# Kernel optimization log

Hardware: AMD Instinct MI355X
Metric: run time of the kernel (lower is better)

## Reference

```python
import jax, jax.numpy as jnp
import numpy as np

HIDDEN = 128
EDGE_DIM = 64
N_NODES = 50000
N_EDGES = 600000

def _linear_params(key, fan_in, fan_out):
    kw, kb = jax.random.split(key)
    bound = 1.0 / np.sqrt(fan_in)
    W = jax.random.uniform(kw, (fan_in, fan_out), minval=-bound, maxval=bound, dtype=jnp.float32)
    b = jax.random.uniform(kb, (fan_out,), minval=-bound, maxval=bound, dtype=jnp.float32)
    return W, b

def setup_inputs() -> dict:
    key = jax.random.key(0)
    ks = jax.random.split(key, 10)
    h = jax.random.normal(ks[0], (N_NODES, HIDDEN), dtype=jnp.float32)
    edge_index = jax.random.randint(ks[1], (2, N_EDGES), 0, N_NODES, dtype=jnp.int64)
    edge_attr = jax.random.normal(ks[2], (N_EDGES, EDGE_DIM), dtype=jnp.float32)
    mW1, mb1 = _linear_params(ks[3], 2 * HIDDEN + EDGE_DIM, HIDDEN)
    mW2, mb2 = _linear_params(ks[4], HIDDEN, HIDDEN)
    mW3, mb3 = _linear_params(ks[5], HIDDEN, HIDDEN)
    uW1, ub1 = _linear_params(ks[6], 2 * HIDDEN, HIDDEN)
    uW2, ub2 = _linear_params(ks[7], HIDDEN, HIDDEN)
    gamma = jnp.ones((HIDDEN,), dtype=jnp.float32)
    beta = jnp.zeros((HIDDEN,), dtype=jnp.float32)
    return {"h": h, "edge_index": edge_index, "edge_attr": edge_attr,
            "mW1": mW1, "mb1": mb1, "mW2": mW2, "mb2": mb2, "mW3": mW3, "mb3": mb3,
            "uW1": uW1, "ub1": ub1, "uW2": uW2, "ub2": ub2,
            "gamma": gamma, "beta": beta}

def reference(h, edge_index, edge_attr, mW1, mb1, mW2, mb2, mW3, mb3, uW1, ub1, uW2, ub2, gamma, beta):
    src, dst = edge_index[0], edge_index[1]
    # message MLP on [E, 2*H + edge_dim]
    x = jnp.concatenate([h[src], h[dst], edge_attr], axis=-1)
    x = jax.nn.gelu(x @ mW1 + mb1)
    x = jax.nn.gelu(x @ mW2 + mb2)
    msgs = x @ mW3 + mb3  # [E, H]
    # scatter-mean aggregate to destination nodes
    agg = jax.ops.segment_sum(msgs, dst, num_segments=h.shape[0])
    count = jax.ops.segment_sum(jnp.ones((dst.shape[0], 1), dtype=h.dtype), dst, num_segments=h.shape[0])
    agg = agg / (count + 1e-8)
    # update MLP
    u = jnp.concatenate([h, agg], axis=-1)
    u = jax.nn.gelu(u @ uW1 + ub1)
    out = u @ uW2 + ub2
    # LayerNorm(out + h)
    y = out + h
    mu = jnp.mean(y, axis=-1, keepdims=True)
    var = jnp.var(y, axis=-1, keepdims=True)
    return (y - mu) / jnp.sqrt(var + 1e-5) * gamma + beta
```

## Files before the change

kernel.cpp:

```cpp
#include <hip/hip_runtime.h>

#define E_TOTAL 600000
#define NN 50000

typedef _Float16 half8 __attribute__((ext_vector_type(8)));
typedef _Float16 half2v __attribute__((ext_vector_type(2)));
typedef float float4v __attribute__((ext_vector_type(4)));
typedef float float2v __attribute__((ext_vector_type(2)));

__device__ __forceinline__ float gelu_tanh(float x) {
    float u = 0.7978845608028654f * (x + 0.044715f * x * x * x);
    float ex = __expf(2.0f * u);
    float t = 1.0f - 2.0f / (ex + 1.0f);
    return 0.5f * x * (1.0f + t);
}

__device__ __forceinline__ int act_idx(int c, int row, int q) {
    int idx = ((c * 128 + row) << 3) + q;
    idx ^= ((row >> 3) & 3) << 4;
    idx ^= (c & 1) << 3;
    return idx;
}
__device__ __forceinline__ int act_idx64(int c, int row, int q) {
    int idx = ((c * 64 + row) << 3) + q;
    idx ^= ((row >> 3) & 3) << 4;
    idx ^= (c & 1) << 3;
    return idx;
}

__device__ __forceinline__ half8 cvt8(float4v x0, float4v x1) {
    half8 a;
    a[0] = (_Float16)x0[0]; a[1] = (_Float16)x0[1]; a[2] = (_Float16)x0[2]; a[3] = (_Float16)x0[3];
    a[4] = (_Float16)x1[0]; a[5] = (_Float16)x1[1]; a[6] = (_Float16)x1[2]; a[7] = (_Float16)x1[3];
    return a;
}

__global__ __launch_bounds__(256) void pack_all(
    const float* __restrict__ mW1, const float* __restrict__ mW2, const float* __restrict__ mW3,
    const float* __restrict__ uW1, const float* __restrict__ uW2,
    _Float16* __restrict__ dst)
{
    int t = blockIdx.x * 256 + threadIdx.x;
    const float* src;
    int loc;
    if (t < 40960)        { src = mW1; loc = t; }
    else if (t < 57344)   { src = mW2; loc = t - 40960; }
    else if (t < 73728)   { src = mW3; loc = t - 57344; }
    else if (t < 106496)  { src = uW1; loc = t - 73728; }
    else if (t < 122880)  { src = uW2; loc = t - 106496; }
    else return;
    int i   = loc & 7;
    int col = (loc >> 3) & 127;
    int c   = loc >> 10;
    dst[t] = (_Float16)src[(8 * c + i) * 128 + col];
}

__global__ __launch_bounds__(256) void cvt_pre(
    const float* __restrict__ h, _Float16* __restrict__ hf)
{
    const int stride = gridDim.x * 256;
    for (int i = blockIdx.x * 256 + threadIdx.x; i < 800000; i += stride) {
        float4v a = ((const float4v*)h)[2 * i];
        float4v b = ((const float4v*)h)[2 * i + 1];
        ((half8*)hf)[i] = cvt8(a, b);
    }
}

__device__ __forceinline__ int detect_i64(const int* ei) {
    int allz = 1;
    #pragma unroll
    for (int j = 1; j < 64; j += 2) allz &= (ei[j] == 0);
    return allz;
}

__global__ __launch_bounds__(256) void count_kernel(const int* __restrict__ ei, int* __restrict__ cnt_i) {
    __shared__ int s_mode;
    if (threadIdx.x == 0) s_mode = detect_i64(ei);
    __syncthreads();
    int e = blockIdx.x * 256 + threadIdx.x;
    if (e >= E_TOTAL) return;
    int d = s_mode ? (int)((const long long*)ei)[E_TOTAL + e] : ei[E_TOTAL + e];
    atomicAdd(&cnt_i[d], 1);
}

__global__ __launch_bounds__(1024) void scan_kernel(const int* __restrict__ cnt_i, int* __restrict__ offs) {
    __shared__ int part[1024];
    const int t = threadIdx.x;
    const int PER = (NN + 1023) / 1024;
    const int base = t * PER;
    int s = 0;
    for (int j = 0; j < PER; ++j) { int idx = base + j; if (idx < NN) s += cnt_i[idx]; }
    part[t] = s;
    __syncthreads();
    for (int off = 1; off < 1024; off <<= 1) {
        int v = (t >= off) ? part[t - off] : 0;
        __syncthreads();
        part[t] += v;
        __syncthreads();
    }
    int run = (t == 0) ? 0 : part[t - 1];
    for (int j = 0; j < PER; ++j) { int idx = base + j; if (idx < NN) { offs[idx] = run; run += cnt_i[idx]; } }
    if (t == 1023) offs[NN] = part[1023];
}

__global__ __launch_bounds__(256) void fill_kernel(const int* __restrict__ ei, const int* __restrict__ offs,
                                                   int* __restrict__ cursor, int* __restrict__ perm) {
    __shared__ int s_mode;
    if (threadIdx.x == 0) s_mode = detect_i64(ei);
    __syncthreads();
    int e = blockIdx.x * 256 + threadIdx.x;
    if (e >= E_TOTAL) return;
    int d = s_mode ? (int)((const long long*)ei)[E_TOTAL + e] : ei[E_TOTAL + e];
    int pos = offs[d] + atomicAdd(&cursor[d], 1);
    perm[pos] = e;
}

__global__ __launch_bounds__(256) void agg_kernel(const _Float16* __restrict__ msgs,
                                                  const int* __restrict__ offs,
                                                  float* __restrict__ agg, float* __restrict__ cntf) {
    const int node = blockIdx.x * 4 + (threadIdx.x >> 6);
    const int l = threadIdx.x & 63;
    const int beg = offs[node], end = offs[node + 1];
    float2v s = {0.0f, 0.0f};
    const half2v* p = (const half2v*)msgs + (size_t)beg * 64 + l;
    int j = beg;
    for (; j + 3 < end; j += 4, p += 256) {
        half2v a = __builtin_nontemporal_load(p);
        half2v b = __builtin_nontemporal_load(p + 64);
        half2v c = __builtin_nontemporal_load(p + 128);
        half2v d = __builtin_nontemporal_load(p + 192);
        s.x += (float)a[0] + (float)b[0] + (float)c[0] + (float)d[0];
        s.y += (float)a[1] + (float)b[1] + (float)c[1] + (float)d[1];
    }
    for (; j < end; ++j, p += 64) {
        half2v v = __builtin_nontemporal_load(p);
        s.x += (float)v[0]; s.y += (float)v[1];
    }
    ((float2v*)agg)[(size_t)node * 64 + l] = s;
    if (l == 0) cntf[node] = (float)(end - beg);
}

template<int ATOMIC>
__global__ __launch_bounds__(128, 3) void msg_kernel(
    const _Float16* __restrict__ hf16, const int* __restrict__ ei, const float* __restrict__ eattr,
    const int* __restrict__ perm,
    const _Float16* __restrict__ pw1, const _Float16* __restrict__ pw2, const _Float16* __restrict__ pw3,
    const float* __restrict__ mb1, const float* __restrict__ mb2, const float* __restrict__ mb3,
    _Float16* __restrict__ msgs, float* __restrict__ agg, float* __restrict__ cnt)
{
    __shared__ int s_e[64];
    __shared__ int s_src[64];
    __shared__ int s_dst[64];
    __shared__ int s_mode;
    __shared__ __align__(16) _Float16 s_act[16 * 64 * 8];

    const int tid = threadIdx.x;
    const int e0  = blockIdx.x * 64;

    if (tid == 0) s_mode = detect_i64(ei);
    __syncthreads();

    if (tid < 64) {
        int e = perm[e0 + tid];
        s_e[tid] = e;
        int srcn, dstn;
        if (s_mode) {
            const long long* e64 = (const long long*)ei;
            srcn = (int)e64[e];
            dstn = (int)e64[E_TOTAL + e];
        } else {
            srcn = ei[e];
            dstn = ei[E_TOTAL + e];
        }
        s_src[tid] = srcn;
        s_dst[tid] = dstn;
        if (ATOMIC) unsafeAtomicAdd(&cnt[dstn], 1.0f);
    }
    __syncthreads();

    const int w = tid >> 6, l = tid & 63, lhi = l >> 4, llo = l & 15;
    const int r0 = 32 * w;
    const float4v fzero = {0.0f, 0.0f, 0.0f, 0.0f};

    const _Float16* srcP[2];
    const _Float16* dstP[2];
    const float*    eP[2];
    #pragma unroll
    for (int ms = 0; ms < 2; ++ms) {
        const int row = r0 + 16 * ms + llo;
        srcP[ms] = hf16 + (size_t)s_src[row] * 128 + 8 * lhi;
        dstP[ms] = hf16 + (size_t)s_dst[row] * 128 + 8 * lhi;
        eP[ms]   = eattr + (size_t)s_e[row] * 64 + 8 * lhi;
    }

    float4v acc[2][8];
    #pragma unroll
    for (int ms = 0; ms < 2; ++ms)
        #pragma unroll
        for (int t = 0; t < 8; ++t) acc[ms][t] = fzero;

    half8 af[4][2];
    #pragma unroll
    for (int s = 0; s < 4; ++s)
        #pragma unroll
        for (int ms = 0; ms < 2; ++ms)
            af[s][ms] = *(const half8*)(srcP[ms] + 32 * s);

    #pragma unroll
    for (int s = 0; s < 10; ++s) {
        const int bbase = ((4 * s + lhi) * 128 + llo) << 3;
        #pragma unroll
        for (int t = 0; t < 8; ++t) {
            const half8 b = *(const half8*)(pw1 + bbase + (t << 7));
            acc[0][t] = __builtin_amdgcn_mfma_f32_16x16x32_f16(af[s & 3][0], b, acc[0][t], 0, 0, 0);
            acc[1][t] = __builtin_amdgcn_mfma_f32_16x16x32_f16(af[s & 3][1], b, acc[1][t], 0, 0, 0);
        }
        if (s + 4 <= 9) {
            const int sn = s + 4;
            #pragma unroll
            for (int ms = 0; ms < 2; ++ms) {
                if (sn < 8) {
                    af[sn & 3][ms] = *(const half8*)(dstP[ms] + 32 * (sn - 4));
                } else {
                    const float* p = eP[ms] + 32 * (sn - 8);
                    float4v x0 = *(const float4v*)p;
                    float4v x1 = *(const float4v*)(p + 4);
                    af[sn & 3][ms] = cvt8(x0, x1);
                }
            }
        }
    }

    #pragma unroll
    for (int t = 0; t < 8; ++t) {
        const int col = 16 * t + llo;
        const float b1 = mb1[col];
        #pragma unroll
        for (int ms = 0; ms < 2; ++ms)
            #pragma unroll
            for (int i = 0; i < 4; ++i) {
                const int row = r0 + 16 * ms + 4 * lhi + i;
                float v = gelu_tanh(acc[ms][t][i] + b1);
                s_act[act_idx64(col >> 3, row, col & 7)] = (_Float16)v;
            }
    }

    float4v acc2[2][8];
    #pragma unroll
    for (int ms = 0; ms < 2; ++ms)
        #pragma unroll
        for (int t = 0; t < 8; ++t) acc2[ms][t] = fzero;

    #pragma unroll
    for (int s = 0; s < 4; ++s) {
        half8 a2[2];
        #pragma unroll
        for (int ms = 0; ms < 2; ++ms)
            a2[ms] = *(const half8*)&s_act[act_idx64(4 * s + lhi, r0 + 16 * ms + llo, 0)];
        const int bbase = ((4 * s + lhi) * 128 + llo) << 3;
        #pragma unroll
        for (int t = 0; t < 8; ++t) {
            const half8 b = *(const half8*)(pw2 + bbase + (t << 7));
            acc2[0][t] = __builtin_amdgcn_mfma_f32_16x16x32_f16(a2[0], b, acc2[0][t], 0, 0, 0);
            acc2[1][t] = __builtin_amdgcn_mfma_f32_16x16x32_f16(a2[1], b, acc2[1][t], 0, 0, 0);
        }
    }

    #pragma unroll
    for (int t = 0; t < 8; ++t) {
        const int col = 16 * t + llo;
        const float b2 = mb2[col];
        #pragma unroll
        for (int ms = 0; ms < 2; ++ms)
            #pragma unroll
            for (int i = 0; i < 4; ++i) {
                const int row = r0 + 16 * ms + 4 * lhi + i;
                float v = gelu_tanh(acc2[ms][t][i] + b2);
                s_act[act_idx64(col >> 3, row, col & 7)] = (_Float16)v;
            }
    }

    float4v acc3[2][8];
    #pragma unroll
    for (int ms = 0; ms < 2; ++ms)
        #pragma unroll
        for (int t = 0; t < 8; ++t) acc3[ms][t] = fzero;

    #pragma unroll
    for (int s = 0; s < 4; ++s) {
        half8 a3[2];
        #pragma unroll
        for (int ms = 0; ms < 2; ++ms)
            a3[ms] = *(const half8*)&s_act[act_idx64(4 * s + lhi, r0 + 16 * ms + llo, 0)];
        const int bbase = ((4 * s + lhi) * 128 + llo) << 3;
        #pragma unroll
        for (int t = 0; t < 8; ++t) {
            const half8 b = *(const half8*)(pw3 + bbase + (t << 7));
            acc3[0][t] = __builtin_amdgcn_mfma_f32_16x16x32_f16(a3[0], b, acc3[0][t], 0, 0, 0);
            acc3[1][t] = __builtin_amdgcn_mfma_f32_16x16x32_f16(a3[1], b, acc3[1][t], 0, 0, 0);
        }
    }

    float mb3v[8];
    #pragma unroll
    for (int t = 0; t < 8; ++t) mb3v[t] = mb3[16 * t + llo];

    #pragma unroll
    for (int ms = 0; ms < 2; ++ms)
        #pragma unroll
        for (int i = 0; i < 4; ++i) {
            const int row = r0 + 16 * ms + 4 * lhi + i;
            if (ATOMIC) {
                const size_t dbase = (size_t)s_dst[row] * 128;
                #pragma unroll
                for (int t = 0; t < 8; ++t)
                    unsafeAtomicAdd(&agg[dbase + 16 * t + llo], acc3[ms][t][i] + mb3v[t]);
            } else {
                _Float16* mrow = msgs + (size_t)(e0 + row) * 128;
                #pragma unroll
                for (int t = 0; t < 8; ++t)
                    __builtin_nontemporal_store((_Float16)(acc3[ms][t][i] + mb3v[t]), mrow + 16 * t + llo);
            }
        }
}

__global__ __launch_bounds__(256) void upd_kernel(
    const float* __restrict__ h, const _Float16* __restrict__ hf16,
    const _Float16* __restrict__ pu1, const _Float16* __restrict__ pu2,
    const float* __restrict__ ub1, const float* __restrict__ ub2,
    const float* __restrict__ gamma, const float* __restrict__ beta,
    const float* __restrict__ agg, const float* __restrict__ cnt,
    float* __restrict__ out)
{
    __shared__ __align__(16) _Float16 s_act[16 * 128 * 8];

    const int tid = threadIdx.x;
    const int n0  = blockIdx.x * 128;
    const int w = tid >> 6, l = tid & 63, lhi = l >> 4, llo = l & 15;
    const int r0 = 32 * w;
    const float4v fzero = {0.0f, 0.0f, 0.0f, 0.0f};

    float rcp[2];
    size_t nodeOff[2];
    #pragma unroll
    for (int ms = 0; ms < 2; ++ms) {
        int node = n0 + r0 + 16 * ms + llo;
        if (node >= NN) node = NN - 1;
        nodeOff[ms] = (size_t)node * 128;
        rcp[ms] = 1.0f / (cnt[node] + 1e-8f);
    }

    float4v acc[2][8];
    #pragma unroll
    for (int ms = 0; ms < 2; ++ms)
        #pragma unroll
        for (int t = 0; t < 8; ++t) acc[ms][t] = fzero;

    #pragma unroll
    for (int s = 0; s < 8; ++s) {
        half8 af[2];
        #pragma unroll
        for (int ms = 0; ms < 2; ++ms) {
            if (s < 4) {
                af[ms] = *(const half8*)(hf16 + nodeOff[ms] + 32 * s + 8 * lhi);
            } else {
                const float* p = agg + nodeOff[ms] + 32 * (s - 4) + 8 * lhi;
                float4v x0 = *(const float4v*)p;
                float4v x1 = *(const float4v*)(p + 4);
                x0 *= rcp[ms]; x1 *= rcp[ms];
                af[ms] = cvt8(x0, x1);
            }
        }
        const int bbase = ((4 * s + lhi) * 128 + llo) << 3;
        #pragma unroll
        for (int t = 0; t < 8; ++t) {
            const half8 b = *(const half8*)(pu1 + bbase + (t << 7));
            acc[0][t] = __builtin_amdgcn_mfma_f32_16x16x32_f16(af[0], b, acc[0][t], 0, 0, 0);
            acc[1][t] = __builtin_amdgcn_mfma_f32_16x16x32_f16(af[1], b, acc[1][t], 0, 0, 0);
        }
    }

    #pragma unroll
    for (int t = 0; t < 8; ++t) {
        const int col = 16 * t + llo;
        const float b1 = ub1[col];
        #pragma unroll
        for (int ms = 0; ms < 2; ++ms)
            #pragma unroll
            for (int i = 0; i < 4; ++i) {
                const int row = r0 + 16 * ms + 4 * lhi + i;
                float v = gelu_tanh(acc[ms][t][i] + b1);
                s_act[act_idx(col >> 3, row, col & 7)] = (_Float16)v;
            }
    }

    float4v acc2[2][8];
    #pragma unroll
    for (int ms = 0; ms < 2; ++ms)
        #pragma unroll
        for (int t = 0; t < 8; ++t) acc2[ms][t] = fzero;

    #pragma unroll
    for (int s = 0; s < 4; ++s) {
        half8 af[2];
        #pragma unroll
        for (int ms = 0; ms < 2; ++ms)
            af[ms] = *(const half8*)&s_act[act_idx(4 * s + lhi, r0 + 16 * ms + llo, 0)];
        const int bbase = ((4 * s + lhi) * 128 + llo) << 3;
        #pragma unroll
        for (int t = 0; t < 8; ++t) {
            const half8 b = *(const half8*)(pu2 + bbase + (t << 7));
            acc2[0][t] = __builtin_amdgcn_mfma_f32_16x16x32_f16(af[0], b, acc2[0][t], 0, 0, 0);
            acc2[1][t] = __builtin_amdgcn_mfma_f32_16x16x32_f16(af[1], b, acc2[1][t], 0, 0, 0);
        }
    }

    float ub2v[8], gv[8], bv[8];
    #pragma unroll
    for (int t = 0; t < 8; ++t) {
        const int col = 16 * t + llo;
        ub2v[t] = ub2[col]; gv[t] = gamma[col]; bv[t] = beta[col];
    }

    #pragma unroll
    for (int ms = 0; ms < 2; ++ms)
        #pragma unroll
        for (int i = 0; i < 4; ++i) {
            const int noderow = n0 + r0 + 16 * ms + 4 * lhi + i;
            const int nodec = noderow < NN ? noderow : NN - 1;
            float y[8];
            float sum = 0.0f;
            #pragma unroll
            for (int t = 0; t < 8; ++t) {
                const int col = 16 * t + llo;
                float v = acc2[ms][t][i] + ub2v[t] + h[(size_t)nodec * 128 + col];
                y[t] = v; sum += v;
            }
            sum += __shfl_xor(sum, 1, 16);
            sum += __shfl_xor(sum, 2, 16);
            sum += __shfl_xor(sum, 4, 16);
            sum += __shfl_xor(sum, 8, 16);
            const float mu = sum * (1.0f / 128.0f);
            float sq = 0.0f;
            #pragma unroll
            for (int t = 0; t < 8; ++t) { float d = y[t] - mu; sq += d * d; }
            sq += __shfl_xor(sq, 1, 16);
            sq += __shfl_xor(sq, 2, 16);
            sq += __shfl_xor(sq, 4, 16);
            sq += __shfl_xor(sq, 8, 16);
            const float rs = rsqrtf(sq * (1.0f / 128.0f) + 1e-5f);
            if (noderow < NN) {
                #pragma unroll
                for (int t = 0; t < 8; ++t) {
                    const int col = 16 * t + llo;
                    out[(size_t)noderow * 128 + col] = (y[t] - mu) * rs * gv[t] + bv[t];
                }
            }
        }
}

extern "C" void kernel_launch(void* const* d_in, const int* in_sizes, int n_in,
                              void* d_out, int out_size, void* d_ws, size_t ws_size,
                              hipStream_t stream) {
    const float* h     = (const float*)d_in[0];
    const int*   ei    = (const int*)d_in[1];
    const float* eattr = (const float*)d_in[2];
    const float* mW1   = (const float*)d_in[3];
    const float* mb1   = (const float*)d_in[4];
    const float* mW2   = (const float*)d_in[5];
    const float* mb2   = (const float*)d_in[6];
    const float* mW3   = (const float*)d_in[7];
    const float* mb3   = (const float*)d_in[8];
    const float* uW1   = (const float*)d_in[9];
    const float* ub1   = (const float*)d_in[10];
    const float* uW2   = (const float*)d_in[11];
    const float* ub2   = (const float*)d_in[12];
    const float* gamma = (const float*)d_in[13];
    const float* beta  = (const float*)d_in[14];
    float* out = (float*)d_out;

    char* ws = (char*)d_ws;

    const size_t OFF_MSGS = 0;
    const size_t OFF_AGG  = 153600000;
    const size_t OFF_HF   = 179200000;
    const size_t OFF_CNTI = 192000000;
    const size_t OFF_CURS = 192200000;
    const size_t OFF_OFFS = 192400000;
    const size_t OFF_PERM = 192600064;
    const size_t OFF_CNTF = 195000064;
    const size_t OFF_PW   = 195200064;
    const size_t NEED     = 195445824;

    if (ws_size >= NEED) {
        _Float16* msgs  = (_Float16*)(ws + OFF_MSGS);
        float* agg      = (float*)(ws + OFF_AGG);
        _Float16* hf16  = (_Float16*)(ws + OFF_HF);
        int* cnt_i      = (int*)(ws + OFF_CNTI);
        int* cursor     = (int*)(ws + OFF_CURS);
        int* offs       = (int*)(ws + OFF_OFFS);
        int* perm       = (int*)(ws + OFF_PERM);
        float* cntf     = (float*)(ws + OFF_CNTF);
        _Float16* pw    = (_Float16*)(ws + OFF_PW);
        _Float16* pw1 = pw;
        _Float16* pw2 = pw + 40960;
        _Float16* pw3 = pw + 57344;
        _Float16* pu1 = pw + 73728;
        _Float16* pu2 = pw + 106496;

        hipMemsetAsync(ws + OFF_CNTI, 0, 400000, stream);

        count_kernel<<<(E_TOTAL + 255) / 256, 256, 0, stream>>>(ei, cnt_i);
        scan_kernel<<<1, 1024, 0, stream>>>(cnt_i, offs);
        fill_kernel<<<(E_TOTAL + 255) / 256, 256, 0, stream>>>(ei, offs, cursor, perm);
        pack_all<<<480, 256, 0, stream>>>(mW1, mW2, mW3, uW1, uW2, pw);
        cvt_pre<<<1024, 256, 0, stream>>>(h, hf16);

        msg_kernel<0><<<E_TOTAL / 64, 128, 0, stream>>>(
            hf16, ei, eattr, perm, pw1, pw2, pw3, mb1, mb2, mb3, msgs, nullptr, nullptr);

        agg_kernel<<<NN / 4, 256, 0, stream>>>(msgs, offs, agg, cntf);

        upd_kernel<<<(NN + 127) / 128, 256, 0, stream>>>(
            h, hf16, pu1, pu2, ub1, ub2, gamma, beta, agg, cntf, out);
    } else {
        float* agg     = (float*)ws;
        float* cnt     = (float*)(ws + 25600000);
        _Float16* hf16 = (_Float16*)(ws + 25800000);
        int* cnt_i     = (int*)(ws + 38600000);
        int* cursor    = (int*)(ws + 38800000);
        int* offs      = (int*)(ws + 39000000);
        int* perm      = (int*)(ws + 39200064);
        _Float16* pw   = (_Float16*)(ws + 41600064);
        _Float16* pw1 = pw;
        _Float16* pw2 = pw + 40960;
        _Float16* pw3 = pw + 57344;
        _Float16* pu1 = pw + 73728;
        _Float16* pu2 = pw + 106496;

        hipMemsetAsync(ws, 0, 25800000, stream);
        hipMemsetAsync(ws + 38600000, 0, 400000, stream);

        count_kernel<<<(E_TOTAL + 255) / 256, 256, 0, stream>>>(ei, cnt_i);
        scan_kernel<<<1, 1024, 0, stream>>>(cnt_i, offs);
        fill_kernel<<<(E_TOTAL + 255) / 256, 256, 0, stream>>>(ei, offs, cursor, perm);
        pack_all<<<480, 256, 0, stream>>>(mW1, mW2, mW3, uW1, uW2, pw);
        cvt_pre<<<1024, 256, 0, stream>>>(h, hf16);

        msg_kernel<1><<<E_TOTAL / 64, 128, 0, stream>>>(
            hf16, ei, eattr, perm, pw1, pw2, pw3, mb1, mb2, mb3, nullptr, agg, cnt);

        upd_kernel<<<(NN + 127) / 128, 256, 0, stream>>>(
            h, hf16, pu1, pu2, ub1, ub2, gamma, beta, agg, cnt, out);
    }
}
```

Baseline: 755.5 us.

## Fuse segment-mean aggregation into update kernel, merge prep kernels, cheaper GELU

Removes the separate aggregation kernel: the update kernel now reads each node's CSR-sorted message rows directly, sums them in registers, and scales by the inverse count before the first update GEMM. This drops the fp32 agg write and read and one launch. The weight-pack and h-to-fp16 conversion kernels are merged into one grid-stride kernel. GELU is rewritten in an algebraically equivalent form using an FMA and a hardware reciprocal. The trade-off is that update threads loop serially over variable-length edge segments, giving per-lane imbalance and less memory parallelism than the dedicated aggregation kernel had.

Result: faster. 716.6 us (-5.2%).

```diff
diff --git a/kernel.cpp b/kernel.cpp
--- a/kernel.cpp
+++ b/kernel.cpp
@@ -9,10 +9,12 @@
 typedef float float2v __attribute__((ext_vector_type(2)));
 
 __device__ __forceinline__ float gelu_tanh(float x) {
-    float u = 0.7978845608028654f * (x + 0.044715f * x * x * x);
-    float ex = __expf(2.0f * u);
-    float t = 1.0f - 2.0f / (ex + 1.0f);
-    return 0.5f * x * (1.0f + t);
+    const float A = 1.5957691216057308f;
+    const float B = 0.0713548163f;
+    float z = x * __builtin_fmaf(B, x * x, A);
+    float ex = __expf(z);
+    float r = __builtin_amdgcn_rcpf(ex + 1.0f);
+    return __builtin_fmaf(-x, r, x);
 }
 
 __device__ __forceinline__ int act_idx(int c, int row, int q) {
@@ -35,34 +37,32 @@
     return a;
 }
 
-__global__ __launch_bounds__(256) void pack_all(
+__global__ __launch_bounds__(256) void prep_kernel(
     const float* __restrict__ mW1, const float* __restrict__ mW2, const float* __restrict__ mW3,
     const float* __restrict__ uW1, const float* __restrict__ uW2,
-    _Float16* __restrict__ dst)
-{
-    int t = blockIdx.x * 256 + threadIdx.x;
-    const float* src;
-    int loc;
-    if (t < 40960)        { src = mW1; loc = t; }
-    else if (t < 57344)   { src = mW2; loc = t - 40960; }
-    else if (t < 73728)   { src = mW3; loc = t - 57344; }
-    else if (t < 106496)  { src = uW1; loc = t - 73728; }
-    else if (t < 122880)  { src = uW2; loc = t - 106496; }
-    else return;
-    int i   = loc & 7;
-    int col = (loc >> 3) & 127;
-    int c   = loc >> 10;
-    dst[t] = (_Float16)src[(8 * c + i) * 128 + col];
-}
-
-__global__ __launch_bounds__(256) void cvt_pre(
-    const float* __restrict__ h, _Float16* __restrict__ hf)
+    const float* __restrict__ h,
+    _Float16* __restrict__ pw, _Float16* __restrict__ hf)
 {
     const int stride = gridDim.x * 256;
-    for (int i = blockIdx.x * 256 + threadIdx.x; i < 800000; i += stride) {
-        float4v a = ((const float4v*)h)[2 * i];
-        float4v b = ((const float4v*)h)[2 * i + 1];
-        ((half8*)hf)[i] = cvt8(a, b);
+    for (int t = blockIdx.x * 256 + threadIdx.x; t < 922880; t += stride) {
+        if (t < 122880) {
+            const float* src;
+            int loc;
+            if (t < 40960)        { src = mW1; loc = t; }
+            else if (t < 57344)   { src = mW2; loc = t - 40960; }
+            else if (t < 73728)   { src = mW3; loc = t - 57344; }
+            else if (t < 106496)  { src = uW1; loc = t - 73728; }
+            else                  { src = uW2; loc = t - 106496; }
+            int i   = loc & 7;
+            int col = (loc >> 3) & 127;
+            int c   = loc >> 10;
+            pw[t] = (_Float16)src[(8 * c + i) * 128 + col];
+        } else {
+            int i = t - 122880;
+            float4v a = ((const float4v*)h)[2 * i];
+            float4v b = ((const float4v*)h)[2 * i + 1];
+            ((half8*)hf)[i] = cvt8(a, b);
+        }
     }
 }
 
@@ -115,31 +115,6 @@
     perm[pos] = e;
 }
 
-__global__ __launch_bounds__(256) void agg_kernel(const _Float16* __restrict__ msgs,
-                                                  const int* __restrict__ offs,
-                                                  float* __restrict__ agg, float* __restrict__ cntf) {
-    const int node = blockIdx.x * 4 + (threadIdx.x >> 6);
-    const int l = threadIdx.x & 63;
-    const int beg = offs[node], end = offs[node + 1];
-    float2v s = {0.0f, 0.0f};
-    const half2v* p = (const half2v*)msgs + (size_t)beg * 64 + l;
-    int j = beg;
-    for (; j + 3 < end; j += 4, p += 256) {
-        half2v a = __builtin_nontemporal_load(p);
-        half2v b = __builtin_nontemporal_load(p + 64);
-        half2v c = __builtin_nontemporal_load(p + 128);
-        half2v d = __builtin_nontemporal_load(p + 192);
-        s.x += (float)a[0] + (float)b[0] + (float)c[0] + (float)d[0];
-        s.y += (float)a[1] + (float)b[1] + (float)c[1] + (float)d[1];
-    }
-    for (; j < end; ++j, p += 64) {
-        half2v v = __builtin_nontemporal_load(p);
-        s.x += (float)v[0]; s.y += (float)v[1];
-    }
-    ((float2v*)agg)[(size_t)node * 64 + l] = s;
-    if (l == 0) cntf[node] = (float)(end - beg);
-}
-
 template<int ATOMIC>
 __global__ __launch_bounds__(128, 3) void msg_kernel(
     const _Float16* __restrict__ hf16, const int* __restrict__ ei, const float* __restrict__ eattr,
@@ -324,8 +299,10 @@
         }
 }
 
+template<int FUSED>
 __global__ __launch_bounds__(256) void upd_kernel(
     const float* __restrict__ h, const _Float16* __restrict__ hf16,
+    const _Float16* __restrict__ msgs, const int* __restrict__ offs,
     const _Float16* __restrict__ pu1, const _Float16* __restrict__ pu2,
     const float* __restrict__ ub1, const float* __restrict__ ub2,
     const float* __restrict__ gamma, const float* __restrict__ beta,
@@ -342,12 +319,46 @@
 
     float rcp[2];
     size_t nodeOff[2];
+    int beg[2], end[2];
     #pragma unroll
     for (int ms = 0; ms < 2; ++ms) {
         int node = n0 + r0 + 16 * ms + llo;
         if (node >= NN) node = NN - 1;
         nodeOff[ms] = (size_t)node * 128;
-        rcp[ms] = 1.0f / (cnt[node] + 1e-8f);
+        if (FUSED) {
+            beg[ms] = offs[node]; end[ms] = offs[node + 1];
+            rcp[ms] = 1.0f / ((float)(end[ms] - beg[ms]) + 1e-8f);
+        } else {
+            rcp[ms] = 1.0f / (cnt[node] + 1e-8f);
+        }
+    }
+
+    half8 afA[2][4];
+    if (FUSED) {
+        #pragma unroll
+        for (int ms = 0; ms < 2; ++ms) {
+            float msum[4][8];
+            #pragma unroll
+            for (int s = 0; s < 4; ++s)
+                #pragma unroll
+                for (int j = 0; j < 8; ++j) msum[s][j] = 0.0f;
+            for (int r = beg[ms]; r < end[ms]; ++r) {
+                const half8* rp = (const half8*)(msgs + (size_t)r * 128) + lhi;
+                #pragma unroll
+                for (int s = 0; s < 4; ++s) {
+                    half8 v = __builtin_nontemporal_load(rp + 4 * s);
+                    #pragma unroll
+                    for (int j = 0; j < 8; ++j) msum[s][j] += (float)v[j];
+                }
+            }
+            #pragma unroll
+            for (int s = 0; s < 4; ++s) {
+                half8 a;
+                #pragma unroll
+                for (int j = 0; j < 8; ++j) a[j] = (_Float16)(msum[s][j] * rcp[ms]);
+                afA[ms][s] = a;
+            }
+        }
     }
 
     float4v acc[2][8];
@@ -363,6 +374,8 @@
         for (int ms = 0; ms < 2; ++ms) {
             if (s < 4) {
                 af[ms] = *(const half8*)(hf16 + nodeOff[ms] + 32 * s + 8 * lhi);
+            } else if (FUSED) {
+                af[ms] = afA[ms][s - 4];
             } else {
                 const float* p = agg + nodeOff[ms] + 32 * (s - 4) + 8 * lhi;
                 float4v x0 = *(const float4v*)p;
@@ -482,25 +495,21 @@
     char* ws = (char*)d_ws;
 
     const size_t OFF_MSGS = 0;
-    const size_t OFF_AGG  = 153600000;
-    const size_t OFF_HF   = 179200000;
-    const size_t OFF_CNTI = 192000000;
-    const size_t OFF_CURS = 192200000;
-    const size_t OFF_OFFS = 192400000;
-    const size_t OFF_PERM = 192600064;
-    const size_t OFF_CNTF = 195000064;
-    const size_t OFF_PW   = 195200064;
-    const size_t NEED     = 195445824;
+    const size_t OFF_HF   = 153600000;
+    const size_t OFF_CNTI = 166400000;
+    const size_t OFF_CURS = 166600000;
+    const size_t OFF_OFFS = 166800000;
+    const size_t OFF_PERM = 167000064;
+    const size_t OFF_PW   = 169400064;
+    const size_t NEED     = 169645824;
 
     if (ws_size >= NEED) {
         _Float16* msgs  = (_Float16*)(ws + OFF_MSGS);
-        float* agg      = (float*)(ws + OFF_AGG);
         _Float16* hf16  = (_Float16*)(ws + OFF_HF);
         int* cnt_i      = (int*)(ws + OFF_CNTI);
         int* cursor     = (int*)(ws + OFF_CURS);
         int* offs       = (int*)(ws + OFF_OFFS);
         int* perm       = (int*)(ws + OFF_PERM);
-        float* cntf     = (float*)(ws + OFF_CNTF);
         _Float16* pw    = (_Float16*)(ws + OFF_PW);
         _Float16* pw1 = pw;
         _Float16* pw2 = pw + 40960;
@@ -513,16 +522,13 @@
         count_kernel<<<(E_TOTAL + 255) / 256, 256, 0, stream>>>(ei, cnt_i);
         scan_kernel<<<1, 1024, 0, stream>>>(cnt_i, offs);
         fill_kernel<<<(E_TOTAL + 255) / 256, 256, 0, stream>>>(ei, offs, cursor, perm);
-        pack_all<<<480, 256, 0, stream>>>(mW1, mW2, mW3, uW1, uW2, pw);
-        cvt_pre<<<1024, 256, 0, stream>>>(h, hf16);
+        prep_kernel<<<1024, 256, 0, stream>>>(mW1, mW2, mW3, uW1, uW2, h, pw, hf16);
 
         msg_kernel<0><<<E_TOTAL / 64, 128, 0, stream>>>(
             hf16, ei, eattr, perm, pw1, pw2, pw3, mb1, mb2, mb3, msgs, nullptr, nullptr);
 
-        agg_kernel<<<NN / 4, 256, 0, stream>>>(msgs, offs, agg, cntf);
-
-        upd_kernel<<<(NN + 127) / 128, 256, 0, stream>>>(
-            h, hf16, pu1, pu2, ub1, ub2, gamma, beta, agg, cntf, out);
+        upd_kernel<1><<<(NN + 127) / 128, 256, 0, stream>>>(
+            h, hf16, msgs, offs, pu1, pu2, ub1, ub2, gamma, beta, nullptr, nullptr, out);
     } else {
         float* agg     = (float*)ws;
         float* cnt     = (float*)(ws + 25600000);
@@ -544,13 +550,12 @@
         count_kernel<<<(E_TOTAL + 255) / 256, 256, 0, stream>>>(ei, cnt_i);
         scan_kernel<<<1, 1024, 0, stream>>>(cnt_i, offs);
         fill_kernel<<<(E_TOTAL + 255) / 256, 256, 0, stream>>>(ei, offs, cursor, perm);
-        pack_all<<<480, 256, 0, stream>>>(mW1, mW2, mW3, uW1, uW2, pw);
-        cvt_pre<<<1024, 256, 0, stream>>>(h, hf16);
+        prep_kernel<<<1024, 256, 0, stream>>>(mW1, mW2, mW3, uW1, uW2, h, pw, hf16);
 
         msg_kernel<1><<<E_TOTAL / 64, 128, 0, stream>>>(
             hf16, ei, eattr, perm, pw1, pw2, pw3, mb1, mb2, mb3, nullptr, agg, cnt);
 
-        upd_kernel<<<(NN + 127) / 128, 256, 0, stream>>>(
-            h, hf16, pu1, pu2, ub1, ub2, gamma, beta, agg, cnt, out);
-    }
-}
+        upd_kernel<0><<<(NN + 127) / 128, 256, 0, stream>>>(
+            h, hf16, nullptr, nullptr, pu1, pu2, ub1, ub2, gamma, beta, agg, cnt, out);
+    }
+}
```
